# Performance work log

Measured on AMD Instinct MI355X. Metric: run time of the kernel, lower is better.

The kernel has to match this reference:

```python
import jax, jax.numpy as jnp
import numpy as np
from functools import partial

H = 64  # hidden_size
F = 5   # num_features
ALPHA_RANK = 1.0
NEG_SLOPE = 0.2


def setup_inputs() -> dict:
    key = jax.random.key(0)
    ks = jax.random.split(key, 10)
    N, T = 4096, 512
    feature = jax.random.normal(ks[0], (N, T, F), dtype=jnp.float32)
    ret = jax.random.normal(ks[1], (N,), dtype=jnp.float32)
    mask = jax.random.bernoulli(ks[2], 0.9, (N,))
    s = 1.0 / np.sqrt(H)
    Wih = jax.random.uniform(ks[3], (4 * H, F), jnp.float32, -s, s)
    Whh = jax.random.uniform(ks[4], (4 * H, H), jnp.float32, -s, s)
    bih = jax.random.uniform(ks[5], (4 * H,), jnp.float32, -s, s)
    bhh = jax.random.uniform(ks[6], (4 * H,), jnp.float32, -s, s)
    Wd = jax.random.uniform(ks[7], (1, H), jnp.float32, -s, s)
    bd = jax.random.uniform(ks[8], (1,), jnp.float32, -s, s)
    return {"feature": feature, "ret": ret, "mask": mask,
            "Wih": Wih, "Whh": Whh, "bih": bih, "bhh": bhh,
            "Wd": Wd, "bd": bd}


def _lstm_last_h(x, Wih, Whh, bih, bhh):
    # x: [N, T, F] -> last hidden state [N, H]. PyTorch gate order: i, f, g, o.
    N = x.shape[0]
    b = bih + bhh
    # precompute input projections for all steps: [T, N, 4H]
    x_proj = jnp.einsum('ntf,gf->tng', x, Wih) + b

    def step(carry, xt):
        h, c = carry
        gates = xt + h @ Whh.T  # [N, 4H]
        i, f, g, o = jnp.split(gates, 4, axis=-1)
        i = jax.nn.sigmoid(i)
        f = jax.nn.sigmoid(f)
        g = jnp.tanh(g)
        o = jax.nn.sigmoid(o)
        c = f * c + i * g
        h = o * jnp.tanh(c)
        return (h, c), None

    h0 = jnp.zeros((N, H), x.dtype)
    c0 = jnp.zeros((N, H), x.dtype)
    (h, _), _ = jax.lax.scan(step, (h0, c0), x_proj)
    return h


def _masked_mse(pred, gt, mask):
    m = mask.astype(pred.dtype)
    return jnp.sum((pred - gt) ** 2 * m) / (jnp.sum(m) + 1e-8)


def _rank_loss(pred, gt, mask):
    m = mask.astype(pred.dtype)
    pred_diff = pred[None, :] - pred[:, None]   # [i,j] = pred[j]-pred[i]
    true_diff = gt[None, :] - gt[:, None]
    mm = m[None, :] * m[:, None]
    return jnp.mean(jax.nn.relu(-pred_diff * true_diff * mm))


def reference(feature, ret, mask, Wih, Whh, bih, bhh, Wd, bd):
    h_last = _lstm_last_h(feature, Wih, Whh, bih, bhh)          # [N, H]
    pred = jax.nn.leaky_relu(h_last @ Wd.T + bd, NEG_SLOPE)[:, 0]  # [N]
    reg_loss = _masked_mse(pred, ret, mask)
    rank_loss = _rank_loss(pred, ret, mask)
    loss = reg_loss + ALPHA_RANK * rank_loss
    return pred, loss, reg_loss, rank_loss
```

## Files before the change

### kernel.cpp

```cpp
#include <hip/hip_runtime.h>

#define NSEQ   4096
#define TSTEPS 512
#define FIN    5
#define HID    64
#define SPB    16
#define BLK    512

typedef __attribute__((ext_vector_type(8))) short bsh8;
typedef __attribute__((ext_vector_type(4))) float f32x4;
typedef __attribute__((ext_vector_type(4))) int   i32x4;

#define MFMA16(A, B, C) __builtin_amdgcn_mfma_f32_16x16x32_bf16((A), (B), (C), 0, 0, 0)

#define LOG2E 1.4426950408889634f
#define SNEG  (-LOG2E)
#define SPOS  (2.0f * LOG2E)

struct Frag2 { bsh8 hi; bsh8 lo; };

__device__ __forceinline__ unsigned short bf16hi_rn(float x) {
    unsigned u = __float_as_uint(x);
    return (unsigned short)((u + 0x7fffu + ((u >> 16) & 1u)) >> 16);
}
__device__ __forceinline__ void split_bf16(float v, unsigned short& h, unsigned short& l) {
    h = bf16hi_rn(v);
    float hf_ = __uint_as_float(((unsigned)h) << 16);
    l = bf16hi_rn(v - hf_);
}

__device__ __forceinline__ Frag2 load_whh_frag(const float* __restrict__ Whh, int row, int k, float scale) {
    const float* p = Whh + row * HID + k;
    Frag2 r;
#pragma unroll
    for (int j = 0; j < 8; ++j) {
        unsigned short h, l;
        split_bf16(scale * p[j], h, l);
        r.hi[j] = (short)h; r.lo[j] = (short)l;
    }
    return r;
}
__device__ __forceinline__ Frag2 load_wih_frag(const float* __restrict__ Wih,
                                               const float* __restrict__ bih,
                                               const float* __restrict__ bhh,
                                               int row, int quad, float scale) {
    Frag2 r;
#pragma unroll
    for (int j = 0; j < 8; ++j) { r.hi[j] = 0; r.lo[j] = 0; }
    if (quad == 0) {
        unsigned short h, l;
#pragma unroll
        for (int j = 0; j < FIN; ++j) {
            split_bf16(scale * Wih[row * FIN + j], h, l);
            r.hi[j] = (short)h; r.lo[j] = (short)l;
        }
        split_bf16(scale * (bih[row] + bhh[row]), h, l);
        r.hi[FIN] = (short)h; r.lo[FIN] = (short)l;
    }
    return r;
}

__device__ __forceinline__ void stage_chunk(const float* __restrict__ feat,
                                            bsh8 (*dst)[SPB],
                                            int seq0, int t0, int tidE) {
#pragma unroll
    for (int it = 0; it < (64 * SPB) / 256; ++it) {
        int idx = tidE + it * 256;
        int t2  = idx >> 4;
        int s   = idx & 15;
        const float* xp = feat + (size_t)(seq0 + s) * (TSTEPS * FIN) + (t0 + t2) * FIN;
        bsh8 v = {0, 0, 0, 0, 0, 0, 0, 0};
#pragma unroll
        for (int j = 0; j < FIN; ++j) v[j] = (short)bf16hi_rn(xp[j]);
        v[FIN] = (short)0x3F80;
        dst[t2][s] = v;
    }
}

__global__ __launch_bounds__(BLK)
void lstm_kernel(const float* __restrict__ feat,
                 const float* __restrict__ Wih,
                 const float* __restrict__ Whh,
                 const float* __restrict__ bih,
                 const float* __restrict__ bhh,
                 const float* __restrict__ Wd,
                 const float* __restrict__ bd,
                 float* __restrict__ pred,
                 float* __restrict__ accums) {
    __shared__ bsh8  aA[2][SPB][9];
    __shared__ bsh8  xb[2][64][SPB];
    __shared__ __align__(16) f32x4 seedb[2][4][4][64];
    __shared__ float hf[SPB][HID + 1];
    __shared__ float pf[SPB][17];

    const int tid   = threadIdx.x;
    const int w     = tid >> 6;
    const int lane  = tid & 63;
    const int col   = lane & 15;
    const int quad  = lane >> 4;
    const int quad4 = quad * 4;
    const int seq0  = blockIdx.x * SPB;

    if (blockIdx.x == 0 && tid < 4) accums[tid] = 0.0f;

    {
        bsh8 z = {0, 0, 0, 0, 0, 0, 0, 0};
        if (tid < SPB * 9) (&aA[0][0][0])[tid] = z;
    }
    if (w >= 4) stage_chunk(feat, xb[0], seq0, 0, tid - 256);
    __syncthreads();

    if (w < 4) {
        const int u = 16 * w + col;
        const Frag2 b00 = load_whh_frag(Whh, 0*HID + u,      quad*8, SNEG);
        const Frag2 b01 = load_whh_frag(Whh, 0*HID + u, 32 + quad*8, SNEG);
        const Frag2 b10 = load_whh_frag(Whh, 1*HID + u,      quad*8, SNEG);
        const Frag2 b11 = load_whh_frag(Whh, 1*HID + u, 32 + quad*8, SNEG);
        const Frag2 b20 = load_whh_frag(Whh, 2*HID + u,      quad*8, SPOS);
        const Frag2 b21 = load_whh_frag(Whh, 2*HID + u, 32 + quad*8, SPOS);
        const Frag2 b30 = load_whh_frag(Whh, 3*HID + u,      quad*8, SNEG);
        const Frag2 b31 = load_whh_frag(Whh, 3*HID + u, 32 + quad*8, SNEG);

        float cs_[4] = {0.f, 0.f, 0.f, 0.f};
        __builtin_amdgcn_s_setprio(1);

        for (int t = 0; t < TSTEPS; ++t) {
            const int buf = t & 1;
            const int nb  = buf ^ 1;
            __syncthreads();

            bsh8 ah0 = aA[buf][col][quad];
            bsh8 ah1 = aA[buf][col][4 + quad];
            f32x4 s0 = seedb[buf][w][0][lane];
            f32x4 s1 = seedb[buf][w][1][lane];
            f32x4 s2 = seedb[buf][w][2][lane];
            f32x4 s3 = seedb[buf][w][3][lane];

            const f32x4 zz = {0.f, 0.f, 0.f, 0.f};
            f32x4 acc0 = MFMA16(ah0, b00.hi, zz);
            f32x4 acc1 = MFMA16(ah0, b10.hi, zz);
            f32x4 acc2 = MFMA16(ah0, b20.hi, zz);
            f32x4 acc3 = MFMA16(ah0, b30.hi, zz);
            acc0 = MFMA16(ah1, b01.hi, acc0);
            acc1 = MFMA16(ah1, b11.hi, acc1);
            acc2 = MFMA16(ah1, b21.hi, acc2);
            acc3 = MFMA16(ah1, b31.hi, acc3);
            acc0 = MFMA16(ah0, b00.lo, acc0);
            acc1 = MFMA16(ah0, b10.lo, acc1);
            acc2 = MFMA16(ah0, b20.lo, acc2);
            acc3 = MFMA16(ah0, b30.lo, acc3);
            acc0 = MFMA16(ah1, b01.lo, acc0);
            acc1 = MFMA16(ah1, b11.lo, acc1);
            acc2 = MFMA16(ah1, b21.lo, acc2);
            acc3 = MFMA16(ah1, b31.lo, acc3);
            acc0 = acc0 + s0;
            acc1 = acc1 + s1;
            acc2 = acc2 + s2;
            acc3 = acc3 + s3;

            float hh_[4];
#pragma unroll
            for (int r = 0; r < 4; ++r) {
                float Ei = __builtin_amdgcn_exp2f(acc0[r]);
                float Ef = __builtin_amdgcn_exp2f(acc1[r]);
                float Eg = __builtin_amdgcn_exp2f(acc2[r]);
                float Eo = __builtin_amdgcn_exp2f(acc3[r]);
                float R1 = __builtin_amdgcn_rcpf((1.0f + Ei) * (1.0f + Eg));
                float sf = __builtin_amdgcn_rcpf(1.0f + Ef);
                float n1 = __builtin_fmaf(SPOS, Eg, -SPOS);
                cs_[r] = __builtin_fmaf(sf, cs_[r], n1 * R1);
                float Ec = __builtin_amdgcn_exp2f(cs_[r]);
                float R2 = __builtin_amdgcn_rcpf((1.0f + Eo) * (1.0f + Ec));
                hh_[r] = (Ec - 1.0f) * R2;
            }
            unsigned pk01, pk23;
            asm("v_cvt_pk_bf16_f32 %0, %1, %2" : "=v"(pk01) : "v"(hh_[0]), "v"(hh_[1]));
            asm("v_cvt_pk_bf16_f32 %0, %1, %2" : "=v"(pk23) : "v"(hh_[2]), "v"(hh_[3]));
            unsigned short* hp = (unsigned short*)&aA[nb][quad4][0] + u;
            hp[0]   = (unsigned short)pk01;
            hp[72]  = (unsigned short)(pk01 >> 16);
            hp[144] = (unsigned short)pk23;
            hp[216] = (unsigned short)(pk23 >> 16);
            if (t == TSTEPS - 1) {
                hf[quad4 + 0][u] = hh_[0];
                hf[quad4 + 1][u] = hh_[1];
                hf[quad4 + 2][u] = hh_[2];
                hf[quad4 + 3][u] = hh_[3];
            }
        }
        __builtin_amdgcn_s_setprio(0);
    } else {
        const int wE   = w - 4;
        const int tidE = tid - 256;
        const int uE   = 16 * wE + col;
        const Frag2 w0 = load_wih_frag(Wih, bih, bhh, 0*HID + uE, quad, SNEG);
        const Frag2 w1 = load_wih_frag(Wih, bih, bhh, 1*HID + uE, quad, SNEG);
        const Frag2 w2 = load_wih_frag(Wih, bih, bhh, 2*HID + uE, quad, SPOS);
        const Frag2 w3 = load_wih_frag(Wih, bih, bhh, 3*HID + uE, quad, SNEG);

        {
            bsh8 ax = xb[0][0][col];
            f32x4 e0 = {0.f,0.f,0.f,0.f}, e1 = e0, e2 = e0, e3 = e0;
            e0 = MFMA16(ax, w0.hi, e0); e0 = MFMA16(ax, w0.lo, e0);
            e1 = MFMA16(ax, w1.hi, e1); e1 = MFMA16(ax, w1.lo, e1);
            e2 = MFMA16(ax, w2.hi, e2); e2 = MFMA16(ax, w2.lo, e2);
            e3 = MFMA16(ax, w3.hi, e3); e3 = MFMA16(ax, w3.lo, e3);
            seedb[0][wE][0][lane] = e0;
            seedb[0][wE][1][lane] = e1;
            seedb[0][wE][2][lane] = e2;
            seedb[0][wE][3][lane] = e3;
        }
        for (int t = 0; t < TSTEPS; ++t) {
            __syncthreads();
            if ((t & 63) == 0 && t + 64 < TSTEPS)
                stage_chunk(feat, xb[((t >> 6) + 1) & 1], seq0, ((t >> 6) + 1) * 64, tidE);
            if (t + 1 < TSTEPS) {
                const int t1 = t + 1;
                bsh8 ax = xb[(t1 >> 6) & 1][t1 & 63][col];
                f32x4 e0 = {0.f,0.f,0.f,0.f}, e1 = e0, e2 = e0, e3 = e0;
                e0 = MFMA16(ax, w0.hi, e0); e0 = MFMA16(ax, w0.lo, e0);
                e1 = MFMA16(ax, w1.hi, e1); e1 = MFMA16(ax, w1.lo, e1);
                e2 = MFMA16(ax, w2.hi, e2); e2 = MFMA16(ax, w2.lo, e2);
                e3 = MFMA16(ax, w3.hi, e3); e3 = MFMA16(ax, w3.lo, e3);
                const int sb = t1 & 1;
                seedb[sb][wE][0][lane] = e0;
                seedb[sb][wE][1][lane] = e1;
                seedb[sb][wE][2][lane] = e2;
                seedb[sb][wE][3][lane] = e3;
            }
        }
    }
    __syncthreads();

    if (tid < 256) {
        int s  = tid & 15;
        int hq = tid >> 4;
        int j0 = hq * 4;
        float part = hf[s][j0] * Wd[j0] + hf[s][j0 + 1] * Wd[j0 + 1]
                   + hf[s][j0 + 2] * Wd[j0 + 2] + hf[s][j0 + 3] * Wd[j0 + 3];
        pf[s][hq] = part;
    }
    __syncthreads();
    if (tid < SPB) {
        float sum = bd[0];
#pragma unroll
        for (int j = 0; j < 16; ++j) sum += pf[tid][j];
        float p = (sum >= 0.0f) ? sum : 0.2f * sum;
        pred[seq0 + tid] = p;
    }
}

__global__ __launch_bounds__(256)
void loss_kernel(const float* __restrict__ pred,
                 const float* __restrict__ ret,
                 const int* __restrict__ mask,
                 float* __restrict__ accums) {
    __shared__ __align__(16) float sp[NSEQ];
    __shared__ __align__(16) float sg[NSEQ];
    __shared__ __align__(16) float sq[NSEQ];
    __shared__ float wsum[8];
    int tid = threadIdx.x;
    for (int idx = tid; idx < NSEQ / 4; idx += 256) {
        f32x4 p4 = ((const f32x4*)pred)[idx];
        f32x4 g4 = ((const f32x4*)ret)[idx];
        i32x4 m4 = ((const i32x4*)mask)[idx];
        f32x4 q4;
#pragma unroll
        for (int l = 0; l < 4; ++l) q4[l] = m4[l] ? 1.0f : 0.0f;
        *(f32x4*)&sp[idx * 4] = p4;
        *(f32x4*)&sg[idx * 4] = g4;
        *(f32x4*)&sq[idx * 4] = q4;
    }
    __syncthreads();

    if (blockIdx.x == 0) {
        float v = 0.0f, m = 0.0f;
        for (int j = tid; j < NSEQ; j += 256) {
            float mj = sq[j];
            float d  = sp[j] - sg[j];
            v += d * d * mj;
            m += mj;
        }
#pragma unroll
        for (int off = 32; off > 0; off >>= 1) {
            v += __shfl_down(v, off, 64);
            m += __shfl_down(m, off, 64);
        }
        if ((tid & 63) == 0) {
            atomicAdd(&accums[0], v);
            atomicAdd(&accums[1], m);
        }
    }

    int iloc = tid >> 5;
    int jp   = tid & 31;
    int i    = blockIdx.x * 8 + iloc;
    float pi = sp[i], gi = sg[i], qi = sq[i];
    float sum = 0.0f;
    for (int j0 = jp * 4; j0 < NSEQ; j0 += 128) {
        f32x4 p4 = *(const f32x4*)&sp[j0];
        f32x4 g4 = *(const f32x4*)&sg[j0];
        f32x4 q4 = *(const f32x4*)&sq[j0];
#pragma unroll
        for (int l = 0; l < 4; ++l) {
            float t = -(p4[l] - pi) * (g4[l] - gi);
            sum += fmaxf(t, 0.0f) * q4[l];
        }
    }
    sum *= qi;
#pragma unroll
    for (int off = 16; off > 0; off >>= 1) sum += __shfl_down(sum, off, 32);
    if (jp == 0) wsum[iloc] = sum;
    __syncthreads();
    if (tid == 0) {
        float s = wsum[0] + wsum[1] + wsum[2] + wsum[3]
                + wsum[4] + wsum[5] + wsum[6] + wsum[7];
        atomicAdd(&accums[2], s);
    }
}

__global__ void final_kernel(const float* __restrict__ accums,
                             float* __restrict__ out) {
    float reg  = accums[0] / (accums[1] + 1e-8f);
    float rank = accums[2] / 16777216.0f;
    out[NSEQ + 0] = reg + rank;
    out[NSEQ + 1] = reg;
    out[NSEQ + 2] = rank;
}

extern "C" void kernel_launch(void* const* d_in, const int* in_sizes, int n_in,
                              void* d_out, int out_size, void* d_ws, size_t ws_size,
                              hipStream_t stream) {
    const float* feat = (const float*)d_in[0];
    const float* ret  = (const float*)d_in[1];
    const int*   mask = (const int*)d_in[2];
    const float* Wih  = (const float*)d_in[3];
    const float* Whh  = (const float*)d_in[4];
    const float* bih  = (const float*)d_in[5];
    const float* bhh  = (const float*)d_in[6];
    const float* Wd   = (const float*)d_in[7];
    const float* bd   = (const float*)d_in[8];
    float* out    = (float*)d_out;
    float* accums = (float*)d_ws;

    lstm_kernel<<<NSEQ / SPB, BLK, 0, stream>>>(feat, Wih, Whh, bih, bhh,
                                                Wd, bd, out, accums);
    loss_kernel<<<NSEQ / 8, 256, 0, stream>>>(out, ret, mask, accums);
    final_kernel<<<1, 1, 0, stream>>>(accums, out);
}
```

Baseline: 351.1 us.

## Split LSTM gate epilogue across recurrent and input-projection waves

The recurrent waves now compute only rows 0-1 of each MFMA tile's nonlinear epilogue. They hand rows 2-3 of the gate pre-activations through shared memory to the input-projection waves, which finish those rows and write their hidden-state halves. The epilogue also shares one reciprocal across two rows by multiplying denominators. This halves the serial transcendental work per wave on the critical path, at the cost of an extra block barrier per timestep and a slightly different reciprocal rounding.

```diff
diff --git a/kernel.cpp b/kernel.cpp
--- a/kernel.cpp
+++ b/kernel.cpp
@@ -9,6 +9,7 @@
 
 typedef __attribute__((ext_vector_type(8))) short bsh8;
 typedef __attribute__((ext_vector_type(4))) float f32x4;
+typedef __attribute__((ext_vector_type(2))) float f32x2;
 typedef __attribute__((ext_vector_type(4))) int   i32x4;
 
 #define MFMA16(A, B, C) __builtin_amdgcn_mfma_f32_16x16x32_bf16((A), (B), (C), 0, 0, 0)
@@ -75,6 +76,31 @@
         v[FIN] = (short)0x3F80;
         dst[t2][s] = v;
     }
+}
+
+__device__ __forceinline__ void epi2(float zi0, float zf0, float zg0, float zo0,
+                                     float zi1, float zf1, float zg1, float zo1,
+                                     float& cs0, float& cs1, float& h0, float& h1) {
+    float Ei0 = __builtin_amdgcn_exp2f(zi0), Ei1 = __builtin_amdgcn_exp2f(zi1);
+    float Ef0 = __builtin_amdgcn_exp2f(zf0), Ef1 = __builtin_amdgcn_exp2f(zf1);
+    float Eg0 = __builtin_amdgcn_exp2f(zg0), Eg1 = __builtin_amdgcn_exp2f(zg1);
+    float P10 = (1.0f + Ei0) * (1.0f + Eg0), Pf0 = 1.0f + Ef0;
+    float P11 = (1.0f + Ei1) * (1.0f + Eg1), Pf1 = 1.0f + Ef1;
+    float D0 = P10 * Pf0, D1 = P11 * Pf1;
+    float Rp = __builtin_amdgcn_rcpf(D0 * D1);
+    float n10 = __builtin_fmaf(SPOS, Eg0, -SPOS);
+    float n11 = __builtin_fmaf(SPOS, Eg1, -SPOS);
+    float m0 = __builtin_fmaf(P10, cs0, n10 * Pf0);
+    float m1 = __builtin_fmaf(P11, cs1, n11 * Pf1);
+    cs0 = (Rp * D1) * m0;
+    cs1 = (Rp * D0) * m1;
+    float Eo0 = __builtin_amdgcn_exp2f(zo0), Eo1 = __builtin_amdgcn_exp2f(zo1);
+    float Ec0 = __builtin_amdgcn_exp2f(cs0), Ec1 = __builtin_amdgcn_exp2f(cs1);
+    float D20 = (1.0f + Eo0) * (1.0f + Ec0);
+    float D21 = (1.0f + Eo1) * (1.0f + Ec1);
+    float R2p = __builtin_amdgcn_rcpf(D20 * D21);
+    h0 = (Ec0 - 1.0f) * (R2p * D21);
+    h1 = (Ec1 - 1.0f) * (R2p * D20);
 }
 
 __global__ __launch_bounds__(BLK)
@@ -89,7 +115,8 @@
                  float* __restrict__ accums) {
     __shared__ bsh8  aA[2][SPB][9];
     __shared__ bsh8  xb[2][64][SPB];
-    __shared__ __align__(16) f32x4 seedb[2][4][4][64];
+    __shared__ __align__(8) f32x2 sg[2][4][4][64];
+    __shared__ __align__(8) f32x2 mb[4][4][64];
     __shared__ float hf[SPB][HID + 1];
     __shared__ float pf[SPB][17];
 
@@ -121,20 +148,23 @@
         const Frag2 b30 = load_whh_frag(Whh, 3*HID + u,      quad*8, SNEG);
         const Frag2 b31 = load_whh_frag(Whh, 3*HID + u, 32 + quad*8, SNEG);
 
-        float cs_[4] = {0.f, 0.f, 0.f, 0.f};
-        __builtin_amdgcn_s_setprio(1);
+        float cs0 = 0.f, cs1 = 0.f;
+        unsigned short* const aAb = (unsigned short*)&aA[0][0][0];
+        const int rowbase = quad4 * 72 + u;
+        const int aAhalf  = SPB * 9 * 8;
 
         for (int t = 0; t < TSTEPS; ++t) {
             const int buf = t & 1;
             const int nb  = buf ^ 1;
+            __builtin_amdgcn_s_setprio(1);
             __syncthreads();
 
             bsh8 ah0 = aA[buf][col][quad];
             bsh8 ah1 = aA[buf][col][4 + quad];
-            f32x4 s0 = seedb[buf][w][0][lane];
-            f32x4 s1 = seedb[buf][w][1][lane];
-            f32x4 s2 = seedb[buf][w][2][lane];
-            f32x4 s3 = seedb[buf][w][3][lane];
+            f32x2 s0 = sg[buf][w][0][lane];
+            f32x2 s1 = sg[buf][w][1][lane];
+            f32x2 s2 = sg[buf][w][2][lane];
+            f32x2 s3 = sg[buf][w][3][lane];
 
             const f32x4 zz = {0.f, 0.f, 0.f, 0.f};
             f32x4 acc0 = MFMA16(ah0, b00.hi, zz);
@@ -153,42 +183,28 @@
             acc1 = MFMA16(ah1, b11.lo, acc1);
             acc2 = MFMA16(ah1, b21.lo, acc2);
             acc3 = MFMA16(ah1, b31.lo, acc3);
-            acc0 = acc0 + s0;
-            acc1 = acc1 + s1;
-            acc2 = acc2 + s2;
-            acc3 = acc3 + s3;
-
-            float hh_[4];
-#pragma unroll
-            for (int r = 0; r < 4; ++r) {
-                float Ei = __builtin_amdgcn_exp2f(acc0[r]);
-                float Ef = __builtin_amdgcn_exp2f(acc1[r]);
-                float Eg = __builtin_amdgcn_exp2f(acc2[r]);
-                float Eo = __builtin_amdgcn_exp2f(acc3[r]);
-                float R1 = __builtin_amdgcn_rcpf((1.0f + Ei) * (1.0f + Eg));
-                float sf = __builtin_amdgcn_rcpf(1.0f + Ef);
-                float n1 = __builtin_fmaf(SPOS, Eg, -SPOS);
-                cs_[r] = __builtin_fmaf(sf, cs_[r], n1 * R1);
-                float Ec = __builtin_amdgcn_exp2f(cs_[r]);
-                float R2 = __builtin_amdgcn_rcpf((1.0f + Eo) * (1.0f + Ec));
-                hh_[r] = (Ec - 1.0f) * R2;
+
+            mb[w][0][lane] = (f32x2){acc0[2], acc0[3]};
+            mb[w][1][lane] = (f32x2){acc1[2], acc1[3]};
+            mb[w][2][lane] = (f32x2){acc2[2], acc2[3]};
+            mb[w][3][lane] = (f32x2){acc3[2], acc3[3]};
+            __builtin_amdgcn_s_setprio(0);
+            __syncthreads();
+
+            float h0, h1;
+            epi2(acc0[0] + s0.x, acc1[0] + s1.x, acc2[0] + s2.x, acc3[0] + s3.x,
+                 acc0[1] + s0.y, acc1[1] + s1.y, acc2[1] + s2.y, acc3[1] + s3.y,
+                 cs0, cs1, h0, h1);
+            unsigned pk;
+            asm("v_cvt_pk_bf16_f32 %0, %1, %2" : "=v"(pk) : "v"(h0), "v"(h1));
+            unsigned short* hp = aAb + nb * aAhalf + rowbase;
+            hp[0]  = (unsigned short)pk;
+            hp[72] = (unsigned short)(pk >> 16);
+            if (t == TSTEPS - 1) {
+                hf[quad4 + 0][u] = h0;
+                hf[quad4 + 1][u] = h1;
             }
-            unsigned pk01, pk23;
-            asm("v_cvt_pk_bf16_f32 %0, %1, %2" : "=v"(pk01) : "v"(hh_[0]), "v"(hh_[1]));
-            asm("v_cvt_pk_bf16_f32 %0, %1, %2" : "=v"(pk23) : "v"(hh_[2]), "v"(hh_[3]));
-            unsigned short* hp = (unsigned short*)&aA[nb][quad4][0] + u;
-            hp[0]   = (unsigned short)pk01;
-            hp[72]  = (unsigned short)(pk01 >> 16);
-            hp[144] = (unsigned short)pk23;
-            hp[216] = (unsigned short)(pk23 >> 16);
-            if (t == TSTEPS - 1) {
-                hf[quad4 + 0][u] = hh_[0];
-                hf[quad4 + 1][u] = hh_[1];
-                hf[quad4 + 2][u] = hh_[2];
-                hf[quad4 + 3][u] = hh_[3];
-            }
-        }
-        __builtin_amdgcn_s_setprio(0);
+        }
     } else {
         const int wE   = w - 4;
         const int tidE = tid - 256;
@@ -198,6 +214,12 @@
         const Frag2 w2 = load_wih_frag(Wih, bih, bhh, 2*HID + uE, quad, SPOS);
         const Frag2 w3 = load_wih_frag(Wih, bih, bhh, 3*HID + uE, quad, SNEG);
 
+        float cs2 = 0.f, cs3 = 0.f;
+        f32x2 ps0, ps1, ps2, ps3;
+        unsigned short* const aAb = (unsigned short*)&aA[0][0][0];
+        const int rowbase = (quad4 + 2) * 72 + uE;
+        const int aAhalf  = SPB * 9 * 8;
+
         {
             bsh8 ax = xb[0][0][col];
             f32x4 e0 = {0.f,0.f,0.f,0.f}, e1 = e0, e2 = e0, e3 = e0;
@@ -205,16 +227,24 @@
             e1 = MFMA16(ax, w1.hi, e1); e1 = MFMA16(ax, w1.lo, e1);
             e2 = MFMA16(ax, w2.hi, e2); e2 = MFMA16(ax, w2.lo, e2);
             e3 = MFMA16(ax, w3.hi, e3); e3 = MFMA16(ax, w3.lo, e3);
-            seedb[0][wE][0][lane] = e0;
-            seedb[0][wE][1][lane] = e1;
-            seedb[0][wE][2][lane] = e2;
-            seedb[0][wE][3][lane] = e3;
-        }
+            sg[0][wE][0][lane] = (f32x2){e0[0], e0[1]};
+            sg[0][wE][1][lane] = (f32x2){e1[0], e1[1]};
+            sg[0][wE][2][lane] = (f32x2){e2[0], e2[1]};
+            sg[0][wE][3][lane] = (f32x2){e3[0], e3[1]};
+            ps0 = (f32x2){e0[2], e0[3]};
+            ps1 = (f32x2){e1[2], e1[3]};
+            ps2 = (f32x2){e2[2], e2[3]};
+            ps3 = (f32x2){e3[2], e3[3]};
+        }
+
         for (int t = 0; t < TSTEPS; ++t) {
+            const int nb = (t & 1) ^ 1;
             __syncthreads();
+            f32x2 ns0, ns1, ns2, ns3;
+            bool have_ns = (t + 1 < TSTEPS);
             if ((t & 63) == 0 && t + 64 < TSTEPS)
                 stage_chunk(feat, xb[((t >> 6) + 1) & 1], seq0, ((t >> 6) + 1) * 64, tidE);
-            if (t + 1 < TSTEPS) {
+            if (have_ns) {
                 const int t1 = t + 1;
                 bsh8 ax = xb[(t1 >> 6) & 1][t1 & 63][col];
                 f32x4 e0 = {0.f,0.f,0.f,0.f}, e1 = e0, e2 = e0, e3 = e0;
@@ -222,11 +252,34 @@
                 e1 = MFMA16(ax, w1.hi, e1); e1 = MFMA16(ax, w1.lo, e1);
                 e2 = MFMA16(ax, w2.hi, e2); e2 = MFMA16(ax, w2.lo, e2);
                 e3 = MFMA16(ax, w3.hi, e3); e3 = MFMA16(ax, w3.lo, e3);
-                const int sb = t1 & 1;
-                seedb[sb][wE][0][lane] = e0;
-                seedb[sb][wE][1][lane] = e1;
-                seedb[sb][wE][2][lane] = e2;
-                seedb[sb][wE][3][lane] = e3;
+                sg[nb][wE][0][lane] = (f32x2){e0[0], e0[1]};
+                sg[nb][wE][1][lane] = (f32x2){e1[0], e1[1]};
+                sg[nb][wE][2][lane] = (f32x2){e2[0], e2[1]};
+                sg[nb][wE][3][lane] = (f32x2){e3[0], e3[1]};
+                ns0 = (f32x2){e0[2], e0[3]};
+                ns1 = (f32x2){e1[2], e1[3]};
+                ns2 = (f32x2){e2[2], e2[3]};
+                ns3 = (f32x2){e3[2], e3[3]};
+            }
+            __syncthreads();
+
+            f32x2 m0 = mb[wE][0][lane];
+            f32x2 m1 = mb[wE][1][lane];
+            f32x2 m2 = mb[wE][2][lane];
+            f32x2 m3 = mb[wE][3][lane];
+            float h2, h3;
+            epi2(m0.x + ps0.x, m1.x + ps1.x, m2.x + ps2.x, m3.x + ps3.x,
+                 m0.y + ps0.y, m1.y + ps1.y, m2.y + ps2.y, m3.y + ps3.y,
+                 cs2, cs3, h2, h3);
+            unsigned pk;
+            asm("v_cvt_pk_bf16_f32 %0, %1, %2" : "=v"(pk) : "v"(h2), "v"(h3));
+            unsigned short* hp = aAb + nb * aAhalf + rowbase;
+            hp[0]  = (unsigned short)pk;
+            hp[72] = (unsigned short)(pk >> 16);
+            if (have_ns) { ps0 = ns0; ps1 = ns1; ps2 = ns2; ps3 = ns3; }
+            else {
+                hf[quad4 + 2][uE] = h2;
+                hf[quad4 + 3][uE] = h3;
             }
         }
     }
@@ -256,7 +309,7 @@
                  const int* __restrict__ mask,
                  float* __restrict__ accums) {
     __shared__ __align__(16) float sp[NSEQ];
-    __shared__ __align__(16) float sg[NSEQ];
+    __shared__ __align__(16) float sg_[NSEQ];
     __shared__ __align__(16) float sq[NSEQ];
     __shared__ float wsum[8];
     int tid = threadIdx.x;
@@ -268,7 +321,7 @@
 #pragma unroll
         for (int l = 0; l < 4; ++l) q4[l] = m4[l] ? 1.0f : 0.0f;
         *(f32x4*)&sp[idx * 4] = p4;
-        *(f32x4*)&sg[idx * 4] = g4;
+        *(f32x4*)&sg_[idx * 4] = g4;
         *(f32x4*)&sq[idx * 4] = q4;
     }
     __syncthreads();
@@ -277,7 +330,7 @@
         float v = 0.0f, m = 0.0f;
         for (int j = tid; j < NSEQ; j += 256) {
             float mj = sq[j];
-            float d  = sp[j] - sg[j];
+            float d  = sp[j] - sg_[j];
             v += d * d * mj;
             m += mj;
         }
@@ -295,11 +348,11 @@
     int iloc = tid >> 5;
     int jp   = tid & 31;
     int i    = blockIdx.x * 8 + iloc;
-    float pi = sp[i], gi = sg[i], qi = sq[i];
+    float pi = sp[i], gi = sg_[i], qi = sq[i];
     float sum = 0.0f;
     for (int j0 = jp * 4; j0 < NSEQ; j0 += 128) {
         f32x4 p4 = *(const f32x4*)&sp[j0];
-        f32x4 g4 = *(const f32x4*)&sg[j0];
+        f32x4 g4 = *(const f32x4*)&sg_[j0];
         f32x4 q4 = *(const f32x4*)&sq[j0];
 #pragma unroll
         for (int l = 0; l < 4; ++l) {
```

New measurement: 412.3 us. 1.17x slower.
